# Kernel optimization log

Measured on AMD Instinct MI355X. Metric: run time of the kernel, lower is better.

Reference implementation:

```python
import jax, jax.numpy as jnp
import numpy as np

N = 25000      # number of mesh vertices
E = 400000     # number of directed edges (avg degree 16)
H = 192        # hidden width (== input_features)
OUT = 3        # output coordinates
N_HID = 13     # gc1..gc13 (all H->H since input_features == hidden)


def setup_inputs() -> dict:
    key = jax.random.key(0)
    ks = jax.random.split(key, 8)
    features = jax.random.normal(ks[0], (N, H), jnp.float32)
    edge_src = jax.random.randint(ks[1], (E,), 0, N, jnp.int32)
    edge_dst = jax.random.randint(ks[2], (E,), 0, N, jnp.int32)
    edge_weight = jax.random.uniform(ks[3], (E,), jnp.float32)
    Ws = jax.random.normal(ks[4], (N_HID, H, H), jnp.float32) * 0.05
    bs = jax.random.normal(ks[5], (N_HID, H), jnp.float32) * 0.05
    W_out = jax.random.normal(ks[6], (H, OUT), jnp.float32) * 0.05
    b_out = jax.random.normal(ks[7], (OUT,), jnp.float32) * 0.05
    return {"features": features, "edge_src": edge_src, "edge_dst": edge_dst,
            "edge_weight": edge_weight, "Ws": Ws, "bs": bs,
            "W_out": W_out, "b_out": b_out}


def _gcn(x, W, b, edge_src, edge_dst, edge_weight):
    # SimpleGCN: adj @ (x @ W) + b, with sparse adj given as an edge list.
    support = x @ W                                   # [N, F_out]
    msg = edge_weight[:, None] * support[edge_src]    # [E, F_out]
    agg = jax.ops.segment_sum(msg, edge_dst, num_segments=N)
    return agg + b


def reference(features, edge_src, edge_dst, edge_weight, Ws, bs, W_out, b_out):
    gcn = lambda x, W, b: _gcn(x, W, b, edge_src, edge_dst, edge_weight)
    # block 1 (gc1, gc2) with truncated-feature residual
    x = jax.nn.relu(gcn(features, Ws[0], bs[0]))
    x = jax.nn.relu(gcn(x, Ws[1], bs[1]))
    feats = (features[..., :H] + x) / 2.0
    # blocks 2-6: (gc3,gc4) (gc5,gc6) (gc7,gc8) (gc9,gc10) (gc11,gc12)
    for i in range(2, 12, 2):
        x = jax.nn.relu(gcn(feats, Ws[i], bs[i]))
        x = jax.nn.relu(gcn(x, Ws[i + 1], bs[i + 1]))
        feats = (feats + x) / 2.0
    # gc13: single conv + residual
    x = jax.nn.relu(gcn(feats, Ws[12], bs[12]))
    feats = (feats + x) / 2.0
    # gc14: output head
    coords = gcn(feats, W_out, b_out)
    return coords, feats
```

## Files before the change

### kernel.cpp

```cpp
#include <hip/hip_runtime.h>
#include <hip/hip_bf16.h>

#define H 192
#define HH (192*192)
#define NLAYER 13
#define LSTRIDE (2*HH)
#define ASTRIDE 200

typedef unsigned short u16;
typedef unsigned int u32;

typedef __attribute__((ext_vector_type(8))) short short8;
typedef __attribute__((ext_vector_type(4))) float floatx4;

__device__ __forceinline__ u16 f2bf(float f) {
    u32 u = __float_as_uint(f);
    u32 r = (u + 0x7FFFu + ((u >> 16) & 1u)) >> 16;
    return (u16)r;
}
__device__ __forceinline__ float bf2f(u16 h) {
    return __uint_as_float(((u32)h) << 16);
}


__global__ void hist2_kernel(const int* __restrict__ src, const int* __restrict__ dst,
                             int* __restrict__ counts2, int E, int t1, int t2) {
    int e = blockIdx.x * blockDim.x + threadIdx.x;
    if (e < E) {
        int s = src[e];
        int r = (s >= t2) ? 2 : ((s >= t1) ? 1 : 0);
        atomicAdd(&counts2[dst[e] * 4 + r], 1);
    }
}

__global__ void alloc2_kernel(const int* __restrict__ counts2, int* __restrict__ rbeg,
                              int* __restrict__ rcnt, int* __restrict__ cursor,
                              int* __restrict__ total, int Nv) {
    int v = blockIdx.x * blockDim.x + threadIdx.x;
    if (v >= Nv) return;
    int c0 = counts2[v * 4 + 0];
    int c1 = counts2[v * 4 + 1];
    int c2 = counts2[v * 4 + 2];
    int tot = c0 + c1 + c2;
    int base = atomicAdd(total, tot);
    rbeg[v] = base;
    rcnt[v] = tot;
    cursor[v * 4 + 0] = base;
    cursor[v * 4 + 1] = base + c0;
    cursor[v * 4 + 2] = base + c0 + c1;
}

__global__ void scatter2_kernel(const int* __restrict__ src, const int* __restrict__ dst,
                                const float* __restrict__ w, int* __restrict__ cursor,
                                int2* __restrict__ ce, int E, int t1, int t2) {
    int e = blockIdx.x * blockDim.x + threadIdx.x;
    if (e < E) {
        int s = src[e];
        int r = (s >= t2) ? 2 : ((s >= t1) ? 1 : 0);
        int p = atomicAdd(&cursor[dst[e] * 4 + r], 1);
        int2 pk; pk.x = s; pk.y = __float_as_int(w[e]);
        ce[p] = pk;
    }
}


__global__ void wprep_kernel(const float* __restrict__ W, u16* __restrict__ Wf, int total) {
    int idx = blockIdx.x * blockDim.x + threadIdx.x;
    if (idx >= total) return;
    int l = idx / HH;
    int rem = idx - l * HH;
    int k = rem / H;
    int n = rem - k * H;
    float v = W[idx];
    u16 hi = f2bf(v);
    u16 lo = f2bf(v - bf2f(hi));
    int ks = k >> 5, quad = (k >> 3) & 3, j = k & 7;
    int nt = n >> 4, col = n & 15;
    int lane = quad * 16 + col;
    size_t base = (size_t)l * LSTRIDE + (size_t)(ks * 12 + nt) * 1024 + lane * 8 + j;
    Wf[base] = hi;
    Wf[base + 512] = lo;
}


__global__ void conv_kernel(const float* __restrict__ in, u16* __restrict__ out, int total4) {
    int idx = blockIdx.x * blockDim.x + threadIdx.x;
    if (idx >= total4) return;
    float4 v = ((const float4*)in)[idx];
    ushort4 p;
    p.x = f2bf(v.x); p.y = f2bf(v.y); p.z = f2bf(v.z); p.w = f2bf(v.w);
    ((ushort4*)out)[idx] = p;
}


__device__ __forceinline__ void fma8(float* acc, uint4 q, float w) {
    u32 u[4] = {q.x, q.y, q.z, q.w};
    #pragma unroll
    for (int i = 0; i < 4; i++) {
        float lo = __uint_as_float(u[i] << 16);
        float hi = __uint_as_float(u[i] & 0xFFFF0000u);
        acc[2*i]     += w * lo;
        acc[2*i + 1] += w * hi;
    }
}


__global__ __launch_bounds__(384) void fused_layer(
    const u16* __restrict__ S, const int* __restrict__ rbeg, const int* __restrict__ rcnt,
    const int2* __restrict__ ce, const u16* __restrict__ Wf, const float* __restrict__ bias,
    u16* __restrict__ out_bf, float* __restrict__ out_f, const u16* __restrict__ resid_bf,
    int mode, int M)
{
    __shared__ u16 shA[16 * ASTRIDE];
    int tid = threadIdx.x;
    int vg = tid / 24;
    int l  = tid - vg * 24;
    int v = blockIdx.x * 16 + vg;

    float acc1[8] = {};
    if (v < M) {
        int beg = rbeg[v], cnt = rcnt[v];
        const int2* cep = ce + beg;
        const u16* Sc = S + l * 8;
        int e = 0;
        for (; e + 3 < cnt; e += 4) {
            int2 p0 = cep[e], p1 = cep[e + 1], p2 = cep[e + 2], p3 = cep[e + 3];
            uint4 q0 = *(const uint4*)(Sc + (size_t)p0.x * H);
            uint4 q1 = *(const uint4*)(Sc + (size_t)p1.x * H);
            uint4 q2 = *(const uint4*)(Sc + (size_t)p2.x * H);
            uint4 q3 = *(const uint4*)(Sc + (size_t)p3.x * H);
            fma8(acc1, q0, __int_as_float(p0.y));
            fma8(acc1, q1, __int_as_float(p1.y));
            fma8(acc1, q2, __int_as_float(p2.y));
            fma8(acc1, q3, __int_as_float(p3.y));
        }
        for (; e < cnt; e++) {
            int2 p0 = cep[e];
            uint4 q0 = *(const uint4*)(Sc + (size_t)p0.x * H);
            fma8(acc1, q0, __int_as_float(p0.y));
        }
    }
    {
        uint4 p;
        p.x = (u32)f2bf(acc1[0]) | ((u32)f2bf(acc1[1]) << 16);
        p.y = (u32)f2bf(acc1[2]) | ((u32)f2bf(acc1[3]) << 16);
        p.z = (u32)f2bf(acc1[4]) | ((u32)f2bf(acc1[5]) << 16);
        p.w = (u32)f2bf(acc1[6]) | ((u32)f2bf(acc1[7]) << 16);
        *(uint4*)&shA[vg * ASTRIDE + l * 8] = p;
    }
    __syncthreads();

    int wave = tid >> 6, lane = tid & 63;
    int col = lane & 15, quad = lane >> 4;

    short8 a[6];
    {
        const u16* Ar = &shA[col * ASTRIDE + quad * 8];
        #pragma unroll
        for (int ks = 0; ks < 6; ks++) a[ks] = *(const short8*)(Ar + ks * 32);
    }

    int nt0 = wave, nt1 = wave + 6;
    floatx4 c0 = {0.f, 0.f, 0.f, 0.f}, c1 = {0.f, 0.f, 0.f, 0.f};
    #pragma unroll
    for (int ks = 0; ks < 6; ks++) {
        const u16* g0 = Wf + (size_t)(ks * 12 + nt0) * 1024 + lane * 8;
        const u16* g1 = Wf + (size_t)(ks * 12 + nt1) * 1024 + lane * 8;
        short8 bh0 = *(const short8*)g0;
        short8 bl0 = *(const short8*)(g0 + 512);
        short8 bh1 = *(const short8*)g1;
        short8 bl1 = *(const short8*)(g1 + 512);
        c0 = __builtin_amdgcn_mfma_f32_16x16x32_bf16(a[ks], bh0, c0, 0, 0, 0);
        c0 = __builtin_amdgcn_mfma_f32_16x16x32_bf16(a[ks], bl0, c0, 0, 0, 0);
        c1 = __builtin_amdgcn_mfma_f32_16x16x32_bf16(a[ks], bh1, c1, 0, 0, 0);
        c1 = __builtin_amdgcn_mfma_f32_16x16x32_bf16(a[ks], bl1, c1, 0, 0, 0);
    }

    int rm = blockIdx.x * 16;
    #pragma unroll
    for (int half = 0; half < 2; half++) {
        int nt = half ? nt1 : nt0;
        floatx4 cc = half ? c1 : c0;
        int n = nt * 16 + col;
        float b = bias[n];
        #pragma unroll
        for (int r = 0; r < 4; r++) {
            int row = rm + quad * 4 + r;
            if (row < M) {
                float z = fmaxf(cc[r] + b, 0.f);
                size_t o = (size_t)row * H + n;
                if (mode >= 1) {
                    float f = (bf2f(resid_bf[o]) + z) * 0.5f;
                    out_bf[o] = f2bf(f);
                    if (mode == 2) out_f[o] = f;
                } else {
                    out_bf[o] = f2bf(z);
                }
            }
        }
    }
}


__global__ __launch_bounds__(192) void spmm_raw(
    const u16* __restrict__ S, const int* __restrict__ rbeg, const int* __restrict__ rcnt,
    const int2* __restrict__ ce, u16* __restrict__ out, int Nv)
{
    int tid = threadIdx.x;
    int g = tid / 24;
    int l = tid - g * 24;
    int v = blockIdx.x * 8 + g;
    if (v >= Nv) return;
    int beg = rbeg[v], cnt = rcnt[v];
    const int2* cep = ce + beg;
    const u16* Sc = S + l * 8;
    float acc[8] = {};
    int e = 0;
    for (; e + 3 < cnt; e += 4) {
        int2 p0 = cep[e], p1 = cep[e + 1], p2 = cep[e + 2], p3 = cep[e + 3];
        uint4 q0 = *(const uint4*)(Sc + (size_t)p0.x * H);
        uint4 q1 = *(const uint4*)(Sc + (size_t)p1.x * H);
        uint4 q2 = *(const uint4*)(Sc + (size_t)p2.x * H);
        uint4 q3 = *(const uint4*)(Sc + (size_t)p3.x * H);
        fma8(acc, q0, __int_as_float(p0.y));
        fma8(acc, q1, __int_as_float(p1.y));
        fma8(acc, q2, __int_as_float(p2.y));
        fma8(acc, q3, __int_as_float(p3.y));
    }
    for (; e < cnt; e++) {
        int2 p0 = cep[e];
        uint4 q0 = *(const uint4*)(Sc + (size_t)p0.x * H);
        fma8(acc, q0, __int_as_float(p0.y));
    }
    size_t idx = (size_t)v * H + l * 8;
    ushort4 o0, o1;
    o0.x = f2bf(acc[0]); o0.y = f2bf(acc[1]); o0.z = f2bf(acc[2]); o0.w = f2bf(acc[3]);
    o1.x = f2bf(acc[4]); o1.y = f2bf(acc[5]); o1.z = f2bf(acc[6]); o1.w = f2bf(acc[7]);
    *(ushort4*)&out[idx] = o0;
    *(ushort4*)&out[idx + 4] = o1;
}


__global__ void head_kernel(const u16* __restrict__ A, const float* __restrict__ W,
                            const float* __restrict__ b, float* __restrict__ coords, int M) {
    int row = blockIdx.x * blockDim.x + threadIdx.x;
    if (row >= M) return;
    float a0 = b[0], a1 = b[1], a2 = b[2];
    const u16* Ar = A + (size_t)row * H;
    for (int k = 0; k < H; k++) {
        float x = bf2f(Ar[k]);
        a0 += x * W[k * 3 + 0];
        a1 += x * W[k * 3 + 1];
        a2 += x * W[k * 3 + 2];
    }
    coords[row * 3 + 0] = a0;
    coords[row * 3 + 1] = a1;
    coords[row * 3 + 2] = a2;
}


extern "C" void kernel_launch(void* const* d_in, const int* in_sizes, int n_in,
                              void* d_out, int out_size, void* d_ws, size_t ws_size,
                              hipStream_t stream) {
    const float* features = (const float*)d_in[0];
    const int*   edge_src = (const int*)d_in[1];
    const int*   edge_dst = (const int*)d_in[2];
    const float* edge_w   = (const float*)d_in[3];
    const float* Ws       = (const float*)d_in[4];
    const float* bs       = (const float*)d_in[5];
    const float* W_out    = (const float*)d_in[6];
    const float* b_out    = (const float*)d_in[7];

    const int N = in_sizes[0] / H;
    const int E = in_sizes[1];
    const int t1 = N / 3, t2 = 2 * N / 3;

    float* coords = (float*)d_out;
    float* feats  = coords + (size_t)N * 3;

    char* wptr = (char*)d_ws;
    u16* fbf  = (u16*)wptr;   wptr += (size_t)N * H * sizeof(u16);
    u16* xb   = (u16*)wptr;   wptr += (size_t)N * H * sizeof(u16);
    u16* fA   = (u16*)wptr;   wptr += (size_t)N * H * sizeof(u16);
    u16* fB   = (u16*)wptr;   wptr += (size_t)N * H * sizeof(u16);
    u16* sup  = (u16*)wptr;   wptr += (size_t)N * H * sizeof(u16);
    u16* Wf   = (u16*)wptr;   wptr += (size_t)NLAYER * LSTRIDE * sizeof(u16);
    int* counts2 = (int*)wptr; wptr += (size_t)N * 4 * sizeof(int);
    int* total   = (int*)wptr; wptr += 4;
    int* rbeg    = (int*)wptr; wptr += (size_t)N * sizeof(int);
    int* rcnt    = (int*)wptr; wptr += (size_t)N * sizeof(int);
    int* cursor  = (int*)wptr; wptr += (size_t)N * 4 * sizeof(int);
    int2* ce     = (int2*)wptr; wptr += (size_t)E * sizeof(int2);

    hipMemsetAsync(counts2, 0, ((size_t)N * 4 + 1) * sizeof(int), stream);
    hist2_kernel<<<(E + 255) / 256, 256, 0, stream>>>(edge_src, edge_dst, counts2, E, t1, t2);
    alloc2_kernel<<<(N + 255) / 256, 256, 0, stream>>>(counts2, rbeg, rcnt, cursor, total, N);
    scatter2_kernel<<<(E + 255) / 256, 256, 0, stream>>>(edge_src, edge_dst, edge_w,
                                                         cursor, ce, E, t1, t2);

    int wtotal = NLAYER * HH;
    wprep_kernel<<<(wtotal + 255) / 256, 256, 0, stream>>>(Ws, Wf, wtotal);
    int c4 = N * H / 4;
    conv_kernel<<<(c4 + 255) / 256, 256, 0, stream>>>(features, fbf, c4);

    int lb = (N + 15) / 16;
    int VC = (N + 7) / 8;

    fused_layer<<<lb, 384, 0, stream>>>(fbf, rbeg, rcnt, ce, Wf + 0 * (size_t)LSTRIDE,
                                        bs + 0 * H, xb, nullptr, nullptr, 0, N);
    fused_layer<<<lb, 384, 0, stream>>>(xb, rbeg, rcnt, ce, Wf + 1 * (size_t)LSTRIDE,
                                        bs + 1 * H, fA, nullptr, fbf, 1, N);

    u16* cur = fA;
    u16* nxt = fB;
    for (int i = 2; i < 12; i += 2) {
        fused_layer<<<lb, 384, 0, stream>>>(cur, rbeg, rcnt, ce, Wf + (size_t)i * LSTRIDE,
                                            bs + (size_t)i * H, xb, nullptr, nullptr, 0, N);
        fused_layer<<<lb, 384, 0, stream>>>(xb, rbeg, rcnt, ce, Wf + (size_t)(i+1) * LSTRIDE,
                                            bs + (size_t)(i+1) * H, nxt, nullptr, cur, 1, N);
        u16* t = cur; cur = nxt; nxt = t;
    }

    fused_layer<<<lb, 384, 0, stream>>>(cur, rbeg, rcnt, ce, Wf + 12 * (size_t)LSTRIDE,
                                        bs + 12 * H, nxt, feats, cur, 2, N);

    spmm_raw<<<VC, 192, 0, stream>>>(nxt, rbeg, rcnt, ce, sup, N);
    head_kernel<<<(N + 255) / 256, 256, 0, stream>>>(sup, W_out, b_out, coords, N);
}
```

Baseline: 604.8 us.

## Split fused layer into column-slab SpMM and register-resident-weight GEMM kernels

```diff
diff --git a/kernel.cpp b/kernel.cpp
--- a/kernel.cpp
+++ b/kernel.cpp
@@ -5,7 +5,8 @@
 #define HH (192*192)
 #define NLAYER 13
 #define LSTRIDE (2*HH)
-#define ASTRIDE 200
+#define VB 128
+#define GR 48
 
 typedef unsigned short u16;
 typedef unsigned int u32;
@@ -23,42 +24,30 @@
 }
 
 
-__global__ void hist2_kernel(const int* __restrict__ src, const int* __restrict__ dst,
-                             int* __restrict__ counts2, int E, int t1, int t2) {
+__global__ void hist_kernel(const int* __restrict__ dst, int* __restrict__ counts, int E) {
+    int e = blockIdx.x * blockDim.x + threadIdx.x;
+    if (e < E) atomicAdd(&counts[dst[e]], 1);
+}
+
+__global__ void alloc_kernel(const int* __restrict__ counts, int* __restrict__ rbeg,
+                             int* __restrict__ rcnt, int* __restrict__ cursor,
+                             int* __restrict__ total, int Nv) {
+    int v = blockIdx.x * blockDim.x + threadIdx.x;
+    if (v >= Nv) return;
+    int cnt = counts[v];
+    int base = atomicAdd(total, cnt);
+    rbeg[v] = base;
+    rcnt[v] = cnt;
+    cursor[v] = base;
+}
+
+__global__ void scatter_kernel(const int* __restrict__ src, const int* __restrict__ dst,
+                               const float* __restrict__ w, int* __restrict__ cursor,
+                               int2* __restrict__ ce, int E) {
     int e = blockIdx.x * blockDim.x + threadIdx.x;
     if (e < E) {
-        int s = src[e];
-        int r = (s >= t2) ? 2 : ((s >= t1) ? 1 : 0);
-        atomicAdd(&counts2[dst[e] * 4 + r], 1);
-    }
-}
-
-__global__ void alloc2_kernel(const int* __restrict__ counts2, int* __restrict__ rbeg,
-                              int* __restrict__ rcnt, int* __restrict__ cursor,
-                              int* __restrict__ total, int Nv) {
-    int v = blockIdx.x * blockDim.x + threadIdx.x;
-    if (v >= Nv) return;
-    int c0 = counts2[v * 4 + 0];
-    int c1 = counts2[v * 4 + 1];
-    int c2 = counts2[v * 4 + 2];
-    int tot = c0 + c1 + c2;
-    int base = atomicAdd(total, tot);
-    rbeg[v] = base;
-    rcnt[v] = tot;
-    cursor[v * 4 + 0] = base;
-    cursor[v * 4 + 1] = base + c0;
-    cursor[v * 4 + 2] = base + c0 + c1;
-}
-
-__global__ void scatter2_kernel(const int* __restrict__ src, const int* __restrict__ dst,
-                                const float* __restrict__ w, int* __restrict__ cursor,
-                                int2* __restrict__ ce, int E, int t1, int t2) {
-    int e = blockIdx.x * blockDim.x + threadIdx.x;
-    if (e < E) {
-        int s = src[e];
-        int r = (s >= t2) ? 2 : ((s >= t1) ? 1 : 0);
-        int p = atomicAdd(&cursor[dst[e] * 4 + r], 1);
-        int2 pk; pk.x = s; pk.y = __float_as_int(w[e]);
+        int p = atomicAdd(&cursor[dst[e]], 1);
+        int2 pk; pk.x = src[e]; pk.y = __float_as_int(w[e]);
         ce[p] = pk;
     }
 }
@@ -105,115 +94,21 @@
 }
 
 
-__global__ __launch_bounds__(384) void fused_layer(
+__global__ __launch_bounds__(384) void spmm_slab(
     const u16* __restrict__ S, const int* __restrict__ rbeg, const int* __restrict__ rcnt,
-    const int2* __restrict__ ce, const u16* __restrict__ Wf, const float* __restrict__ bias,
-    u16* __restrict__ out_bf, float* __restrict__ out_f, const u16* __restrict__ resid_bf,
-    int mode, int M)
+    const int2* __restrict__ ce, u16* __restrict__ agg, int M)
 {
-    __shared__ u16 shA[16 * ASTRIDE];
-    int tid = threadIdx.x;
-    int vg = tid / 24;
-    int l  = tid - vg * 24;
-    int v = blockIdx.x * 16 + vg;
-
-    float acc1[8] = {};
-    if (v < M) {
-        int beg = rbeg[v], cnt = rcnt[v];
-        const int2* cep = ce + beg;
-        const u16* Sc = S + l * 8;
-        int e = 0;
-        for (; e + 3 < cnt; e += 4) {
-            int2 p0 = cep[e], p1 = cep[e + 1], p2 = cep[e + 2], p3 = cep[e + 3];
-            uint4 q0 = *(const uint4*)(Sc + (size_t)p0.x * H);
-            uint4 q1 = *(const uint4*)(Sc + (size_t)p1.x * H);
-            uint4 q2 = *(const uint4*)(Sc + (size_t)p2.x * H);
-            uint4 q3 = *(const uint4*)(Sc + (size_t)p3.x * H);
-            fma8(acc1, q0, __int_as_float(p0.y));
-            fma8(acc1, q1, __int_as_float(p1.y));
-            fma8(acc1, q2, __int_as_float(p2.y));
-            fma8(acc1, q3, __int_as_float(p3.y));
-        }
-        for (; e < cnt; e++) {
-            int2 p0 = cep[e];
-            uint4 q0 = *(const uint4*)(Sc + (size_t)p0.x * H);
-            fma8(acc1, q0, __int_as_float(p0.y));
-        }
-    }
-    {
-        uint4 p;
-        p.x = (u32)f2bf(acc1[0]) | ((u32)f2bf(acc1[1]) << 16);
-        p.y = (u32)f2bf(acc1[2]) | ((u32)f2bf(acc1[3]) << 16);
-        p.z = (u32)f2bf(acc1[4]) | ((u32)f2bf(acc1[5]) << 16);
-        p.w = (u32)f2bf(acc1[6]) | ((u32)f2bf(acc1[7]) << 16);
-        *(uint4*)&shA[vg * ASTRIDE + l * 8] = p;
-    }
-    __syncthreads();
-
-    int wave = tid >> 6, lane = tid & 63;
-    int col = lane & 15, quad = lane >> 4;
-
-    short8 a[6];
-    {
-        const u16* Ar = &shA[col * ASTRIDE + quad * 8];
-        #pragma unroll
-        for (int ks = 0; ks < 6; ks++) a[ks] = *(const short8*)(Ar + ks * 32);
-    }
-
-    int nt0 = wave, nt1 = wave + 6;
-    floatx4 c0 = {0.f, 0.f, 0.f, 0.f}, c1 = {0.f, 0.f, 0.f, 0.f};
-    #pragma unroll
-    for (int ks = 0; ks < 6; ks++) {
-        const u16* g0 = Wf + (size_t)(ks * 12 + nt0) * 1024 + lane * 8;
-        const u16* g1 = Wf + (size_t)(ks * 12 + nt1) * 1024 + lane * 8;
-        short8 bh0 = *(const short8*)g0;
-        short8 bl0 = *(const short8*)(g0 + 512);
-        short8 bh1 = *(const short8*)g1;
-        short8 bl1 = *(const short8*)(g1 + 512);
-        c0 = __builtin_amdgcn_mfma_f32_16x16x32_bf16(a[ks], bh0, c0, 0, 0, 0);
-        c0 = __builtin_amdgcn_mfma_f32_16x16x32_bf16(a[ks], bl0, c0, 0, 0, 0);
-        c1 = __builtin_amdgcn_mfma_f32_16x16x32_bf16(a[ks], bh1, c1, 0, 0, 0);
-        c1 = __builtin_amdgcn_mfma_f32_16x16x32_bf16(a[ks], bl1, c1, 0, 0, 0);
-    }
-
-    int rm = blockIdx.x * 16;
-    #pragma unroll
-    for (int half = 0; half < 2; half++) {
-        int nt = half ? nt1 : nt0;
-        floatx4 cc = half ? c1 : c0;
-        int n = nt * 16 + col;
-        float b = bias[n];
-        #pragma unroll
-        for (int r = 0; r < 4; r++) {
-            int row = rm + quad * 4 + r;
-            if (row < M) {
-                float z = fmaxf(cc[r] + b, 0.f);
-                size_t o = (size_t)row * H + n;
-                if (mode >= 1) {
-                    float f = (bf2f(resid_bf[o]) + z) * 0.5f;
-                    out_bf[o] = f2bf(f);
-                    if (mode == 2) out_f[o] = f;
-                } else {
-                    out_bf[o] = f2bf(z);
-                }
-            }
-        }
-    }
-}
-
-
-__global__ __launch_bounds__(192) void spmm_raw(
-    const u16* __restrict__ S, const int* __restrict__ rbeg, const int* __restrict__ rcnt,
-    const int2* __restrict__ ce, u16* __restrict__ out, int Nv)
-{
-    int tid = threadIdx.x;
-    int g = tid / 24;
-    int l = tid - g * 24;
-    int v = blockIdx.x * 8 + g;
-    if (v >= Nv) return;
+    int slab = blockIdx.x & 7;
+    int vb   = blockIdx.x >> 3;
+    int tid  = threadIdx.x;
+    int vg = tid / 3;
+    int l  = tid - vg * 3;
+    int v = vb * VB + vg;
+    if (v >= M) return;
+
+    const u16* Sc = S + slab * 24 + l * 8;
     int beg = rbeg[v], cnt = rcnt[v];
     const int2* cep = ce + beg;
-    const u16* Sc = S + l * 8;
     float acc[8] = {};
     int e = 0;
     for (; e + 3 < cnt; e += 4) {
@@ -232,12 +127,82 @@
         uint4 q0 = *(const uint4*)(Sc + (size_t)p0.x * H);
         fma8(acc, q0, __int_as_float(p0.y));
     }
-    size_t idx = (size_t)v * H + l * 8;
-    ushort4 o0, o1;
-    o0.x = f2bf(acc[0]); o0.y = f2bf(acc[1]); o0.z = f2bf(acc[2]); o0.w = f2bf(acc[3]);
-    o1.x = f2bf(acc[4]); o1.y = f2bf(acc[5]); o1.z = f2bf(acc[6]); o1.w = f2bf(acc[7]);
-    *(ushort4*)&out[idx] = o0;
-    *(ushort4*)&out[idx + 4] = o1;
+
+    uint4 p;
+    p.x = (u32)f2bf(acc[0]) | ((u32)f2bf(acc[1]) << 16);
+    p.y = (u32)f2bf(acc[2]) | ((u32)f2bf(acc[3]) << 16);
+    p.z = (u32)f2bf(acc[4]) | ((u32)f2bf(acc[5]) << 16);
+    p.w = (u32)f2bf(acc[6]) | ((u32)f2bf(acc[7]) << 16);
+    *(uint4*)&agg[(size_t)v * H + slab * 24 + l * 8] = p;
+}
+
+
+__global__ __launch_bounds__(384) void gemm_layer(
+    const u16* __restrict__ A, const u16* __restrict__ Wf, const float* __restrict__ bias,
+    u16* __restrict__ out_bf, float* __restrict__ out_f, const u16* __restrict__ resid_bf,
+    int mode, int M)
+{
+    int tid = threadIdx.x;
+    int wave = tid >> 6, lane = tid & 63;
+    int col = lane & 15, quad = lane >> 4;
+    int nt0 = wave, nt1 = wave + 6;
+
+    short8 bh0[6], bl0[6], bh1[6], bl1[6];
+    #pragma unroll
+    for (int ks = 0; ks < 6; ks++) {
+        const u16* g0 = Wf + (size_t)(ks * 12 + nt0) * 1024 + lane * 8;
+        const u16* g1 = Wf + (size_t)(ks * 12 + nt1) * 1024 + lane * 8;
+        bh0[ks] = *(const short8*)g0;
+        bl0[ks] = *(const short8*)(g0 + 512);
+        bh1[ks] = *(const short8*)g1;
+        bl1[ks] = *(const short8*)(g1 + 512);
+    }
+
+    int rm0 = blockIdx.x * GR;
+    #pragma unroll
+    for (int t = 0; t < GR / 16; t++) {
+        int rm = rm0 + t * 16;
+        if (rm >= M) break;
+
+        int arow = rm + col;
+        if (arow >= M) arow = M - 1;
+        const u16* Ar = A + (size_t)arow * H + quad * 8;
+        short8 a[6];
+        #pragma unroll
+        for (int ks = 0; ks < 6; ks++) a[ks] = *(const short8*)(Ar + ks * 32);
+
+        floatx4 c0 = {0.f, 0.f, 0.f, 0.f}, c1 = {0.f, 0.f, 0.f, 0.f};
+        #pragma unroll
+        for (int ks = 0; ks < 6; ks++) {
+            c0 = __builtin_amdgcn_mfma_f32_16x16x32_bf16(a[ks], bh0[ks], c0, 0, 0, 0);
+            c0 = __builtin_amdgcn_mfma_f32_16x16x32_bf16(a[ks], bl0[ks], c0, 0, 0, 0);
+            c1 = __builtin_amdgcn_mfma_f32_16x16x32_bf16(a[ks], bh1[ks], c1, 0, 0, 0);
+            c1 = __builtin_amdgcn_mfma_f32_16x16x32_bf16(a[ks], bl1[ks], c1, 0, 0, 0);
+        }
+
+        #pragma unroll
+        for (int half = 0; half < 2; half++) {
+            int nt = half ? nt1 : nt0;
+            floatx4 cc = half ? c1 : c0;
+            int n = nt * 16 + col;
+            float b = bias[n];
+            #pragma unroll
+            for (int r = 0; r < 4; r++) {
+                int row = rm + quad * 4 + r;
+                if (row < M) {
+                    float z = fmaxf(cc[r] + b, 0.f);
+                    size_t o = (size_t)row * H + n;
+                    if (mode >= 1) {
+                        float f = (bf2f(resid_bf[o]) + z) * 0.5f;
+                        out_bf[o] = f2bf(f);
+                        if (mode == 2) out_f[o] = f;
+                    } else {
+                        out_bf[o] = f2bf(z);
+                    }
+                }
+            }
+        }
+    }
 }
 
 
@@ -247,11 +212,17 @@
     if (row >= M) return;
     float a0 = b[0], a1 = b[1], a2 = b[2];
     const u16* Ar = A + (size_t)row * H;
-    for (int k = 0; k < H; k++) {
-        float x = bf2f(Ar[k]);
-        a0 += x * W[k * 3 + 0];
-        a1 += x * W[k * 3 + 1];
-        a2 += x * W[k * 3 + 2];
+    #pragma unroll
+    for (int k8 = 0; k8 < H / 8; k8++) {
+        short8 v = *(const short8*)(Ar + k8 * 8);
+        #pragma unroll
+        for (int j = 0; j < 8; j++) {
+            float x = bf2f((u16)v[j]);
+            int k = k8 * 8 + j;
+            a0 += x * W[k * 3 + 0];
+            a1 += x * W[k * 3 + 1];
+            a2 += x * W[k * 3 + 2];
+        }
     }
     coords[row * 3 + 0] = a0;
     coords[row * 3 + 1] = a1;
@@ -273,7 +244,6 @@
 
     const int N = in_sizes[0] / H;
     const int E = in_sizes[1];
-    const int t1 = N / 3, t2 = 2 * N / 3;
 
     float* coords = (float*)d_out;
     float* feats  = coords + (size_t)N * 3;
@@ -283,47 +253,52 @@
     u16* xb   = (u16*)wptr;   wptr += (size_t)N * H * sizeof(u16);
     u16* fA   = (u16*)wptr;   wptr += (size_t)N * H * sizeof(u16);
     u16* fB   = (u16*)wptr;   wptr += (size_t)N * H * sizeof(u16);
-    u16* sup  = (u16*)wptr;   wptr += (size_t)N * H * sizeof(u16);
+    u16* agg  = (u16*)wptr;   wptr += (size_t)N * H * sizeof(u16);
     u16* Wf   = (u16*)wptr;   wptr += (size_t)NLAYER * LSTRIDE * sizeof(u16);
-    int* counts2 = (int*)wptr; wptr += (size_t)N * 4 * sizeof(int);
-    int* total   = (int*)wptr; wptr += 4;
-    int* rbeg    = (int*)wptr; wptr += (size_t)N * sizeof(int);
-    int* rcnt    = (int*)wptr; wptr += (size_t)N * sizeof(int);
-    int* cursor  = (int*)wptr; wptr += (size_t)N * 4 * sizeof(int);
-    int2* ce     = (int2*)wptr; wptr += (size_t)E * sizeof(int2);
-
-    hipMemsetAsync(counts2, 0, ((size_t)N * 4 + 1) * sizeof(int), stream);
-    hist2_kernel<<<(E + 255) / 256, 256, 0, stream>>>(edge_src, edge_dst, counts2, E, t1, t2);
-    alloc2_kernel<<<(N + 255) / 256, 256, 0, stream>>>(counts2, rbeg, rcnt, cursor, total, N);
-    scatter2_kernel<<<(E + 255) / 256, 256, 0, stream>>>(edge_src, edge_dst, edge_w,
-                                                         cursor, ce, E, t1, t2);
+    int* counts = (int*)wptr; wptr += (size_t)N * sizeof(int);
+    int* total  = (int*)wptr; wptr += 16;
+    int* rbeg   = (int*)wptr; wptr += (size_t)N * sizeof(int);
+    int* rcnt   = (int*)wptr; wptr += (size_t)N * sizeof(int);
+    int* cursor = (int*)wptr; wptr += (size_t)N * sizeof(int);
+    int2* ce    = (int2*)wptr; wptr += (size_t)E * sizeof(int2);
+
+    hipMemsetAsync(counts, 0, (size_t)N * sizeof(int) + 16, stream);
+    hist_kernel<<<(E + 255) / 256, 256, 0, stream>>>(edge_dst, counts, E);
+    alloc_kernel<<<(N + 255) / 256, 256, 0, stream>>>(counts, rbeg, rcnt, cursor, total, N);
+    scatter_kernel<<<(E + 255) / 256, 256, 0, stream>>>(edge_src, edge_dst, edge_w,
+                                                        cursor, ce, E);
 
     int wtotal = NLAYER * HH;
     wprep_kernel<<<(wtotal + 255) / 256, 256, 0, stream>>>(Ws, Wf, wtotal);
     int c4 = N * H / 4;
     conv_kernel<<<(c4 + 255) / 256, 256, 0, stream>>>(features, fbf, c4);
 
-    int lb = (N + 15) / 16;
-    int VC = (N + 7) / 8;
-
-    fused_layer<<<lb, 384, 0, stream>>>(fbf, rbeg, rcnt, ce, Wf + 0 * (size_t)LSTRIDE,
-                                        bs + 0 * H, xb, nullptr, nullptr, 0, N);
-    fused_layer<<<lb, 384, 0, stream>>>(xb, rbeg, rcnt, ce, Wf + 1 * (size_t)LSTRIDE,
-                                        bs + 1 * H, fA, nullptr, fbf, 1, N);
+    int nvb = (N + VB - 1) / VB;
+    int sg  = 8 * nvb;
+    int gb  = (N + GR - 1) / GR;
+
+    spmm_slab<<<sg, 384, 0, stream>>>(fbf, rbeg, rcnt, ce, agg, N);
+    gemm_layer<<<gb, 384, 0, stream>>>(agg, Wf, bs, xb, nullptr, nullptr, 0, N);
+    spmm_slab<<<sg, 384, 0, stream>>>(xb, rbeg, rcnt, ce, agg, N);
+    gemm_layer<<<gb, 384, 0, stream>>>(agg, Wf + (size_t)LSTRIDE, bs + H, fA,
+                                       nullptr, fbf, 1, N);
 
     u16* cur = fA;
     u16* nxt = fB;
     for (int i = 2; i < 12; i += 2) {
-        fused_layer<<<lb, 384, 0, stream>>>(cur, rbeg, rcnt, ce, Wf + (size_t)i * LSTRIDE,
-                                            bs + (size_t)i * H, xb, nullptr, nullptr, 0, N);
-        fused_layer<<<lb, 384, 0, stream>>>(xb, rbeg, rcnt, ce, Wf + (size_t)(i+1) * LSTRIDE,
-                                            bs + (size_t)(i+1) * H, nxt, nullptr, cur, 1, N);
+        spmm_slab<<<sg, 384, 0, stream>>>(cur, rbeg, rcnt, ce, agg, N);
+        gemm_layer<<<gb, 384, 0, stream>>>(agg, Wf + (size_t)i * LSTRIDE, bs + (size_t)i * H,
+                                           xb, nullptr, nullptr, 0, N);
+        spmm_slab<<<sg, 384, 0, stream>>>(xb, rbeg, rcnt, ce, agg, N);
+        gemm_layer<<<gb, 384, 0, stream>>>(agg, Wf + (size_t)(i + 1) * LSTRIDE,
+                                           bs + (size_t)(i + 1) * H, nxt, nullptr, cur, 1, N);
         u16* t = cur; cur = nxt; nxt = t;
     }
 
-    fused_layer<<<lb, 384, 0, stream>>>(cur, rbeg, rcnt, ce, Wf + 12 * (size_t)LSTRIDE,
-                                        bs + 12 * H, nxt, feats, cur, 2, N);
-
-    spmm_raw<<<VC, 192, 0, stream>>>(nxt, rbeg, rcnt, ce, sup, N);
-    head_kernel<<<(N + 255) / 256, 256, 0, stream>>>(sup, W_out, b_out, coords, N);
-}
+    spmm_slab<<<sg, 384, 0, stream>>>(cur, rbeg, rcnt, ce, agg, N);
+    gemm_layer<<<gb, 384, 0, stream>>>(agg, Wf + 12 * (size_t)LSTRIDE, bs + 12 * H,
+                                       nxt, feats, cur, 2, N);
+
+    spmm_slab<<<sg, 384, 0, stream>>>(nxt, rbeg, rcnt, ce, agg, N);
+    head_kernel<<<(N + 255) / 256, 256, 0, stream>>>(agg, W_out, b_out, coords, N);
+}
```

New measurement: 1.345 ms. 122% more time.

## Process 32 vertices per block in fused layer and vectorize head loads

Applied to the files above, without the earlier changes.

```diff
diff --git a/kernel.cpp b/kernel.cpp
--- a/kernel.cpp
+++ b/kernel.cpp
@@ -6,6 +6,7 @@
 #define NLAYER 13
 #define LSTRIDE (2*HH)
 #define ASTRIDE 200
+#define VPB 32
 
 typedef unsigned short u16;
 typedef unsigned int u32;
@@ -111,57 +112,75 @@
     u16* __restrict__ out_bf, float* __restrict__ out_f, const u16* __restrict__ resid_bf,
     int mode, int M)
 {
-    __shared__ u16 shA[16 * ASTRIDE];
+    __shared__ u16 shA[VPB * ASTRIDE];
     int tid = threadIdx.x;
-    int vg = tid / 24;
-    int l  = tid - vg * 24;
-    int v = blockIdx.x * 16 + vg;
-
-    float acc1[8] = {};
+    int vg = tid / 12;
+    int l  = tid - vg * 12;
+    int v = blockIdx.x * VPB + vg;
+
+    float acc[16] = {};
     if (v < M) {
         int beg = rbeg[v], cnt = rcnt[v];
         const int2* cep = ce + beg;
-        const u16* Sc = S + l * 8;
+        const u16* Sc = S + l * 16;
         int e = 0;
         for (; e + 3 < cnt; e += 4) {
             int2 p0 = cep[e], p1 = cep[e + 1], p2 = cep[e + 2], p3 = cep[e + 3];
-            uint4 q0 = *(const uint4*)(Sc + (size_t)p0.x * H);
-            uint4 q1 = *(const uint4*)(Sc + (size_t)p1.x * H);
-            uint4 q2 = *(const uint4*)(Sc + (size_t)p2.x * H);
-            uint4 q3 = *(const uint4*)(Sc + (size_t)p3.x * H);
-            fma8(acc1, q0, __int_as_float(p0.y));
-            fma8(acc1, q1, __int_as_float(p1.y));
-            fma8(acc1, q2, __int_as_float(p2.y));
-            fma8(acc1, q3, __int_as_float(p3.y));
+            const u16* r0 = Sc + (size_t)p0.x * H;
+            const u16* r1 = Sc + (size_t)p1.x * H;
+            const u16* r2 = Sc + (size_t)p2.x * H;
+            const u16* r3 = Sc + (size_t)p3.x * H;
+            uint4 q0a = *(const uint4*)r0, q0b = *(const uint4*)(r0 + 8);
+            uint4 q1a = *(const uint4*)r1, q1b = *(const uint4*)(r1 + 8);
+            uint4 q2a = *(const uint4*)r2, q2b = *(const uint4*)(r2 + 8);
+            uint4 q3a = *(const uint4*)r3, q3b = *(const uint4*)(r3 + 8);
+            float w0 = __int_as_float(p0.y), w1 = __int_as_float(p1.y);
+            float w2 = __int_as_float(p2.y), w3 = __int_as_float(p3.y);
+            fma8(acc, q0a, w0); fma8(acc + 8, q0b, w0);
+            fma8(acc, q1a, w1); fma8(acc + 8, q1b, w1);
+            fma8(acc, q2a, w2); fma8(acc + 8, q2b, w2);
+            fma8(acc, q3a, w3); fma8(acc + 8, q3b, w3);
         }
         for (; e < cnt; e++) {
             int2 p0 = cep[e];
-            uint4 q0 = *(const uint4*)(Sc + (size_t)p0.x * H);
-            fma8(acc1, q0, __int_as_float(p0.y));
+            const u16* r0 = Sc + (size_t)p0.x * H;
+            uint4 qa = *(const uint4*)r0, qb = *(const uint4*)(r0 + 8);
+            float w0 = __int_as_float(p0.y);
+            fma8(acc, qa, w0); fma8(acc + 8, qb, w0);
         }
     }
     {
-        uint4 p;
-        p.x = (u32)f2bf(acc1[0]) | ((u32)f2bf(acc1[1]) << 16);
-        p.y = (u32)f2bf(acc1[2]) | ((u32)f2bf(acc1[3]) << 16);
-        p.z = (u32)f2bf(acc1[4]) | ((u32)f2bf(acc1[5]) << 16);
-        p.w = (u32)f2bf(acc1[6]) | ((u32)f2bf(acc1[7]) << 16);
-        *(uint4*)&shA[vg * ASTRIDE + l * 8] = p;
+        uint4 pa, pb;
+        pa.x = (u32)f2bf(acc[0])  | ((u32)f2bf(acc[1])  << 16);
+        pa.y = (u32)f2bf(acc[2])  | ((u32)f2bf(acc[3])  << 16);
+        pa.z = (u32)f2bf(acc[4])  | ((u32)f2bf(acc[5])  << 16);
+        pa.w = (u32)f2bf(acc[6])  | ((u32)f2bf(acc[7])  << 16);
+        pb.x = (u32)f2bf(acc[8])  | ((u32)f2bf(acc[9])  << 16);
+        pb.y = (u32)f2bf(acc[10]) | ((u32)f2bf(acc[11]) << 16);
+        pb.z = (u32)f2bf(acc[12]) | ((u32)f2bf(acc[13]) << 16);
+        pb.w = (u32)f2bf(acc[14]) | ((u32)f2bf(acc[15]) << 16);
+        *(uint4*)&shA[vg * ASTRIDE + l * 16] = pa;
+        *(uint4*)&shA[vg * ASTRIDE + l * 16 + 8] = pb;
     }
     __syncthreads();
 
     int wave = tid >> 6, lane = tid & 63;
     int col = lane & 15, quad = lane >> 4;
 
-    short8 a[6];
+    short8 a0[6], a1[6];
     {
-        const u16* Ar = &shA[col * ASTRIDE + quad * 8];
+        const u16* Ar0 = &shA[col * ASTRIDE + quad * 8];
+        const u16* Ar1 = &shA[(16 + col) * ASTRIDE + quad * 8];
         #pragma unroll
-        for (int ks = 0; ks < 6; ks++) a[ks] = *(const short8*)(Ar + ks * 32);
+        for (int ks = 0; ks < 6; ks++) {
+            a0[ks] = *(const short8*)(Ar0 + ks * 32);
+            a1[ks] = *(const short8*)(Ar1 + ks * 32);
+        }
     }
 
     int nt0 = wave, nt1 = wave + 6;
-    floatx4 c0 = {0.f, 0.f, 0.f, 0.f}, c1 = {0.f, 0.f, 0.f, 0.f};
+    floatx4 c00 = {0.f, 0.f, 0.f, 0.f}, c01 = {0.f, 0.f, 0.f, 0.f};
+    floatx4 c10 = {0.f, 0.f, 0.f, 0.f}, c11 = {0.f, 0.f, 0.f, 0.f};
     #pragma unroll
     for (int ks = 0; ks < 6; ks++) {
         const u16* g0 = Wf + (size_t)(ks * 12 + nt0) * 1024 + lane * 8;
@@ -170,31 +189,39 @@
         short8 bl0 = *(const short8*)(g0 + 512);
         short8 bh1 = *(const short8*)g1;
         short8 bl1 = *(const short8*)(g1 + 512);
-        c0 = __builtin_amdgcn_mfma_f32_16x16x32_bf16(a[ks], bh0, c0, 0, 0, 0);
-        c0 = __builtin_amdgcn_mfma_f32_16x16x32_bf16(a[ks], bl0, c0, 0, 0, 0);
-        c1 = __builtin_amdgcn_mfma_f32_16x16x32_bf16(a[ks], bh1, c1, 0, 0, 0);
-        c1 = __builtin_amdgcn_mfma_f32_16x16x32_bf16(a[ks], bl1, c1, 0, 0, 0);
-    }
-
-    int rm = blockIdx.x * 16;
+        c00 = __builtin_amdgcn_mfma_f32_16x16x32_bf16(a0[ks], bh0, c00, 0, 0, 0);
+        c00 = __builtin_amdgcn_mfma_f32_16x16x32_bf16(a0[ks], bl0, c00, 0, 0, 0);
+        c10 = __builtin_amdgcn_mfma_f32_16x16x32_bf16(a1[ks], bh0, c10, 0, 0, 0);
+        c10 = __builtin_amdgcn_mfma_f32_16x16x32_bf16(a1[ks], bl0, c10, 0, 0, 0);
+        c01 = __builtin_amdgcn_mfma_f32_16x16x32_bf16(a0[ks], bh1, c01, 0, 0, 0);
+        c01 = __builtin_amdgcn_mfma_f32_16x16x32_bf16(a0[ks], bl1, c01, 0, 0, 0);
+        c11 = __builtin_amdgcn_mfma_f32_16x16x32_bf16(a1[ks], bh1, c11, 0, 0, 0);
+        c11 = __builtin_amdgcn_mfma_f32_16x16x32_bf16(a1[ks], bl1, c11, 0, 0, 0);
+    }
+
+    int rm = blockIdx.x * VPB;
     #pragma unroll
-    for (int half = 0; half < 2; half++) {
-        int nt = half ? nt1 : nt0;
-        floatx4 cc = half ? c1 : c0;
-        int n = nt * 16 + col;
-        float b = bias[n];
+    for (int tile = 0; tile < 2; tile++) {
+        int rbase = rm + tile * 16;
         #pragma unroll
-        for (int r = 0; r < 4; r++) {
-            int row = rm + quad * 4 + r;
-            if (row < M) {
-                float z = fmaxf(cc[r] + b, 0.f);
-                size_t o = (size_t)row * H + n;
-                if (mode >= 1) {
-                    float f = (bf2f(resid_bf[o]) + z) * 0.5f;
-                    out_bf[o] = f2bf(f);
-                    if (mode == 2) out_f[o] = f;
-                } else {
-                    out_bf[o] = f2bf(z);
+        for (int half = 0; half < 2; half++) {
+            int nt = half ? nt1 : nt0;
+            floatx4 cc = tile ? (half ? c11 : c10) : (half ? c01 : c00);
+            int n = nt * 16 + col;
+            float b = bias[n];
+            #pragma unroll
+            for (int r = 0; r < 4; r++) {
+                int row = rbase + quad * 4 + r;
+                if (row < M) {
+                    float z = fmaxf(cc[r] + b, 0.f);
+                    size_t o = (size_t)row * H + n;
+                    if (mode >= 1) {
+                        float f = (bf2f(resid_bf[o]) + z) * 0.5f;
+                        out_bf[o] = f2bf(f);
+                        if (mode == 2) out_f[o] = f;
+                    } else {
+                        out_bf[o] = f2bf(z);
+                    }
                 }
             }
         }
@@ -247,11 +274,17 @@
     if (row >= M) return;
     float a0 = b[0], a1 = b[1], a2 = b[2];
     const u16* Ar = A + (size_t)row * H;
-    for (int k = 0; k < H; k++) {
-        float x = bf2f(Ar[k]);
-        a0 += x * W[k * 3 + 0];
-        a1 += x * W[k * 3 + 1];
-        a2 += x * W[k * 3 + 2];
+    #pragma unroll
+    for (int k8 = 0; k8 < H / 8; k8++) {
+        short8 v = *(const short8*)(Ar + k8 * 8);
+        #pragma unroll
+        for (int j = 0; j < 8; j++) {
+            float x = bf2f((u16)v[j]);
+            int k = k8 * 8 + j;
+            a0 += x * W[k * 3 + 0];
+            a1 += x * W[k * 3 + 1];
+            a2 += x * W[k * 3 + 2];
+        }
     }
     coords[row * 3 + 0] = a0;
     coords[row * 3 + 1] = a1;
@@ -303,7 +336,7 @@
     int c4 = N * H / 4;
     conv_kernel<<<(c4 + 255) / 256, 256, 0, stream>>>(features, fbf, c4);
 
-    int lb = (N + 15) / 16;
+    int lb = (N + VPB - 1) / VPB;
     int VC = (N + 7) / 8;
 
     fused_layer<<<lb, 384, 0, stream>>>(fbf, rbeg, rcnt, ce, Wf + 0 * (size_t)LSTRIDE,
```

New measurement: 719.1 us. 1.19x slower.

## Sort vertices by in-degree to balance SpMM work across wavefronts

Applied to the files above, without the earlier changes.

```diff
diff --git a/kernel.cpp b/kernel.cpp
--- a/kernel.cpp
+++ b/kernel.cpp
@@ -6,6 +6,7 @@
 #define NLAYER 13
 #define LSTRIDE (2*HH)
 #define ASTRIDE 200
+#define DBINS 64
 
 typedef unsigned short u16;
 typedef unsigned int u32;
@@ -60,6 +61,38 @@
         int p = atomicAdd(&cursor[dst[e] * 4 + r], 1);
         int2 pk; pk.x = s; pk.y = __float_as_int(w[e]);
         ce[p] = pk;
+    }
+}
+
+
+__global__ void deg_hist_kernel(const int* __restrict__ rcnt, int* __restrict__ dh, int Nv) {
+    int v = blockIdx.x * blockDim.x + threadIdx.x;
+    if (v < Nv) {
+        int b = rcnt[v]; if (b > DBINS - 1) b = DBINS - 1;
+        atomicAdd(&dh[b], 1);
+    }
+}
+
+__global__ void deg_base_kernel(const int* __restrict__ dh, int* __restrict__ dcur) {
+    __shared__ int s[DBINS];
+    int t = threadIdx.x;
+    s[t] = dh[t];
+    __syncthreads();
+    if (t == 0) {
+        int run = 0;
+        for (int b = DBINS - 1; b >= 0; b--) { int c = s[b]; s[b] = run; run += c; }
+    }
+    __syncthreads();
+    dcur[t] = s[t];
+}
+
+__global__ void deg_scatter_kernel(const int* __restrict__ rcnt, int* __restrict__ dcur,
+                                   int* __restrict__ vmap, int Nv) {
+    int v = blockIdx.x * blockDim.x + threadIdx.x;
+    if (v < Nv) {
+        int b = rcnt[v]; if (b > DBINS - 1) b = DBINS - 1;
+        int p = atomicAdd(&dcur[b], 1);
+        vmap[p] = v;
     }
 }
 
@@ -107,7 +140,8 @@
 
 __global__ __launch_bounds__(384) void fused_layer(
     const u16* __restrict__ S, const int* __restrict__ rbeg, const int* __restrict__ rcnt,
-    const int2* __restrict__ ce, const u16* __restrict__ Wf, const float* __restrict__ bias,
+    const int2* __restrict__ ce, const int* __restrict__ vmap,
+    const u16* __restrict__ Wf, const float* __restrict__ bias,
     u16* __restrict__ out_bf, float* __restrict__ out_f, const u16* __restrict__ resid_bf,
     int mode, int M)
 {
@@ -115,10 +149,11 @@
     int tid = threadIdx.x;
     int vg = tid / 24;
     int l  = tid - vg * 24;
-    int v = blockIdx.x * 16 + vg;
+    int slot = blockIdx.x * 16 + vg;
 
     float acc1[8] = {};
-    if (v < M) {
+    if (slot < M) {
+        int v = vmap[slot];
         int beg = rbeg[v], cnt = rcnt[v];
         const int2* cep = ce + beg;
         const u16* Sc = S + l * 8;
@@ -185,8 +220,9 @@
         float b = bias[n];
         #pragma unroll
         for (int r = 0; r < 4; r++) {
-            int row = rm + quad * 4 + r;
-            if (row < M) {
+            int rslot = rm + quad * 4 + r;
+            if (rslot < M) {
+                int row = vmap[rslot];
                 float z = fmaxf(cc[r] + b, 0.f);
                 size_t o = (size_t)row * H + n;
                 if (mode >= 1) {
@@ -204,13 +240,15 @@
 
 __global__ __launch_bounds__(192) void spmm_raw(
     const u16* __restrict__ S, const int* __restrict__ rbeg, const int* __restrict__ rcnt,
-    const int2* __restrict__ ce, u16* __restrict__ out, int Nv)
+    const int2* __restrict__ ce, const int* __restrict__ vmap,
+    u16* __restrict__ out, int Nv)
 {
     int tid = threadIdx.x;
     int g = tid / 24;
     int l = tid - g * 24;
-    int v = blockIdx.x * 8 + g;
-    if (v >= Nv) return;
+    int slot = blockIdx.x * 8 + g;
+    if (slot >= Nv) return;
+    int v = vmap[slot];
     int beg = rbeg[v], cnt = rcnt[v];
     const int2* cep = ce + beg;
     const u16* Sc = S + l * 8;
@@ -247,11 +285,17 @@
     if (row >= M) return;
     float a0 = b[0], a1 = b[1], a2 = b[2];
     const u16* Ar = A + (size_t)row * H;
-    for (int k = 0; k < H; k++) {
-        float x = bf2f(Ar[k]);
-        a0 += x * W[k * 3 + 0];
-        a1 += x * W[k * 3 + 1];
-        a2 += x * W[k * 3 + 2];
+    #pragma unroll
+    for (int k8 = 0; k8 < H / 8; k8++) {
+        short8 v = *(const short8*)(Ar + k8 * 8);
+        #pragma unroll
+        for (int j = 0; j < 8; j++) {
+            float x = bf2f((u16)v[j]);
+            int k = k8 * 8 + j;
+            a0 += x * W[k * 3 + 0];
+            a1 += x * W[k * 3 + 1];
+            a2 += x * W[k * 3 + 2];
+        }
     }
     coords[row * 3 + 0] = a0;
     coords[row * 3 + 1] = a1;
@@ -291,13 +335,21 @@
     int* rcnt    = (int*)wptr; wptr += (size_t)N * sizeof(int);
     int* cursor  = (int*)wptr; wptr += (size_t)N * 4 * sizeof(int);
     int2* ce     = (int2*)wptr; wptr += (size_t)E * sizeof(int2);
+    int* dh      = (int*)wptr; wptr += DBINS * sizeof(int);
+    int* dcur    = (int*)wptr; wptr += DBINS * sizeof(int);
+    int* vmap    = (int*)wptr; wptr += (size_t)N * sizeof(int);
 
     hipMemsetAsync(counts2, 0, ((size_t)N * 4 + 1) * sizeof(int), stream);
+    hipMemsetAsync(dh, 0, DBINS * sizeof(int), stream);
     hist2_kernel<<<(E + 255) / 256, 256, 0, stream>>>(edge_src, edge_dst, counts2, E, t1, t2);
     alloc2_kernel<<<(N + 255) / 256, 256, 0, stream>>>(counts2, rbeg, rcnt, cursor, total, N);
     scatter2_kernel<<<(E + 255) / 256, 256, 0, stream>>>(edge_src, edge_dst, edge_w,
                                                          cursor, ce, E, t1, t2);
 
+    deg_hist_kernel<<<(N + 255) / 256, 256, 0, stream>>>(rcnt, dh, N);
+    deg_base_kernel<<<1, DBINS, 0, stream>>>(dh, dcur);
+    deg_scatter_kernel<<<(N + 255) / 256, 256, 0, stream>>>(rcnt, dcur, vmap, N);
+
     int wtotal = NLAYER * HH;
     wprep_kernel<<<(wtotal + 255) / 256, 256, 0, stream>>>(Ws, Wf, wtotal);
     int c4 = N * H / 4;
@@ -306,24 +358,26 @@
     int lb = (N + 15) / 16;
     int VC = (N + 7) / 8;
 
-    fused_layer<<<lb, 384, 0, stream>>>(fbf, rbeg, rcnt, ce, Wf + 0 * (size_t)LSTRIDE,
+    fused_layer<<<lb, 384, 0, stream>>>(fbf, rbeg, rcnt, ce, vmap, Wf + 0 * (size_t)LSTRIDE,
                                         bs + 0 * H, xb, nullptr, nullptr, 0, N);
-    fused_layer<<<lb, 384, 0, stream>>>(xb, rbeg, rcnt, ce, Wf + 1 * (size_t)LSTRIDE,
+    fused_layer<<<lb, 384, 0, stream>>>(xb, rbeg, rcnt, ce, vmap, Wf + 1 * (size_t)LSTRIDE,
                                         bs + 1 * H, fA, nullptr, fbf, 1, N);
 
     u16* cur = fA;
     u16* nxt = fB;
     for (int i = 2; i < 12; i += 2) {
-        fused_layer<<<lb, 384, 0, stream>>>(cur, rbeg, rcnt, ce, Wf + (size_t)i * LSTRIDE,
+        fused_layer<<<lb, 384, 0, stream>>>(cur, rbeg, rcnt, ce, vmap,
+                                            Wf + (size_t)i * LSTRIDE,
                                             bs + (size_t)i * H, xb, nullptr, nullptr, 0, N);
-        fused_layer<<<lb, 384, 0, stream>>>(xb, rbeg, rcnt, ce, Wf + (size_t)(i+1) * LSTRIDE,
+        fused_layer<<<lb, 384, 0, stream>>>(xb, rbeg, rcnt, ce, vmap,
+                                            Wf + (size_t)(i+1) * LSTRIDE,
                                             bs + (size_t)(i+1) * H, nxt, nullptr, cur, 1, N);
         u16* t = cur; cur = nxt; nxt = t;
     }
 
-    fused_layer<<<lb, 384, 0, stream>>>(cur, rbeg, rcnt, ce, Wf + 12 * (size_t)LSTRIDE,
+    fused_layer<<<lb, 384, 0, stream>>>(cur, rbeg, rcnt, ce, vmap, Wf + 12 * (size_t)LSTRIDE,
                                         bs + 12 * H, nxt, feats, cur, 2, N);
 
-    spmm_raw<<<VC, 192, 0, stream>>>(nxt, rbeg, rcnt, ce, sup, N);
+    spmm_raw<<<VC, 192, 0, stream>>>(nxt, rbeg, rcnt, ce, vmap, sup, N);
     head_kernel<<<(N + 255) / 256, 256, 0, stream>>>(sup, W_out, b_out, coords, N);
 }
```

Result: slower. 722.2 us (+19.4%).
